# Optimization experiments

Measured on AMD Instinct MI355X. Metric: run time of the kernel, lower is better.

The kernel has to match this reference:

```python
import jax, jax.numpy as jnp
import numpy as np

EPSILON = 0.1      # max offset magnitude relative to anchor norm (init kwarg)
NORM_EPS = 1e-12   # F.normalize denom clamp
DIV_EPS = 1e-8     # offset-norm division eps


def setup_inputs() -> dict:
    key = jax.random.key(0)
    k1, k2 = jax.random.split(key)
    embeddings = jax.random.normal(k1, (4, 2048, 2048), dtype=jnp.float32)
    vocab_embeddings = jax.random.normal(k2, (32000, 2048), dtype=jnp.float32)
    return {"embeddings": embeddings, "vocab_embeddings": vocab_embeddings}


def reference(embeddings, vocab_embeddings):
    B, S, D = embeddings.shape
    x = embeddings.reshape(-1, D)                                   # [BS, D]
    xn = x / jnp.maximum(jnp.linalg.norm(x, axis=-1, keepdims=True), NORM_EPS)
    vn = vocab_embeddings / jnp.maximum(
        jnp.linalg.norm(vocab_embeddings, axis=-1, keepdims=True), NORM_EPS)
    sim = xn @ vn.T                                                 # [BS, V]
    anchor_ids = jnp.argmax(sim, axis=-1)                           # [BS]
    anchor = vocab_embeddings[anchor_ids]                           # [BS, D]
    offset = x - anchor
    offset_norm = jnp.linalg.norm(offset, axis=-1, keepdims=True)
    anchor_norm = jnp.linalg.norm(anchor, axis=-1, keepdims=True)
    scale = jnp.minimum(EPSILON * anchor_norm / (offset_norm + DIV_EPS), 1.0)
    result = anchor + offset * scale
    return result.reshape(B, S, D), anchor_ids.reshape(B, S)
```

## Files before the change

### kernel.cpp

```cpp
#include <hip/hip_runtime.h>
#include <hip/hip_bf16.h>

#define DIM 2048
#define BM 128
#define BN 256
#define BK 64
#define KSTEPS (DIM / BK)
#define A_TILE_BYTES (BM * BK)
#define B_TILE_BYTES (BN * BK)
#define NLEV 8

typedef _Float16 f16x8 __attribute__((ext_vector_type(8)));
typedef float f32x4 __attribute__((ext_vector_type(4)));
typedef int i32x4 __attribute__((ext_vector_type(4)));
typedef unsigned long long u64;

#define INV_SX 27.6f
#define INV_SVN 1150.0f

typedef const unsigned int __attribute__((address_space(1))) gu32;
typedef unsigned int __attribute__((address_space(3))) lu32;

__device__ __forceinline__ void gl_lds16(const void* g, void* l) {
    __builtin_amdgcn_global_load_lds((gu32*)g, (lu32*)l, 16, 0, 0);
}

__device__ __forceinline__ u64 pack_key(float v, unsigned int col) {
    unsigned int b = __float_as_uint(v);
    b ^= (unsigned int)(((int)b >> 31)) | 0x80000000u;
    return ((u64)b << 32) | (u64)(~col);
}
__device__ __forceinline__ u64 pack_key_i(int dot, unsigned int col) {
    unsigned int b = (unsigned int)dot ^ 0x80000000u;
    return ((u64)b << 32) | (u64)(~col);
}
__device__ __forceinline__ u64 umax64(u64 a, u64 b) { return a > b ? a : b; }
__device__ __forceinline__ u64 umin64(u64 a, u64 b) { return a < b ? a : b; }

__device__ __forceinline__ void cascadeN(u64* Rrow, int stride, u64 k) {
    if (k <= Rrow[(NLEV - 1) * stride]) return;
#pragma unroll
    for (int l = 0; l < NLEV; ++l) {
        u64 old = atomicMax(&Rrow[l * stride], k);
        k = umin64(k, old);
        if (!k) return;
    }
}
__device__ __forceinline__ void cascade3(u64* r1, u64* r2, u64* r3, u64 k) {
    u64 old = atomicMax(r1, k);
    k = umin64(k, old);
    if (k) {
        old = atomicMax(r2, k);
        k = umin64(k, old);
        if (k) atomicMax(r3, k);
    }
}

__device__ __forceinline__ int toff(int row, int kg) {
    const int line = row >> 1;
    const int s8 = ((row & 1) << 2) | kg;
    return line * 128 + ((s8 ^ (line & 7)) << 4);
}

__device__ __forceinline__ int swz(int row, int slot) {
    return row * 32 + (slot ^ ((row >> 1) & 3)) * 8;
}

__global__ void vocab_invnorm_kernel(const float* __restrict__ Vg,
                                     float* __restrict__ invnorm) {
    const int v = blockIdx.x;
    const int t = threadIdx.x;
    const float* row = Vg + (size_t)v * DIM;
    float4 f0 = *reinterpret_cast<const float4*>(row + t * 8);
    float4 f1 = *reinterpret_cast<const float4*>(row + t * 8 + 4);
    float s = f0.x*f0.x + f0.y*f0.y + f0.z*f0.z + f0.w*f0.w
            + f1.x*f1.x + f1.y*f1.y + f1.z*f1.z + f1.w*f1.w;
#pragma unroll
    for (int off = 32; off > 0; off >>= 1) s += __shfl_down(s, off);
    __shared__ float ls[4];
    const int lane = t & 63, w = t >> 6;
    if (lane == 0) ls[w] = s;
    __syncthreads();
    if (t == 0) {
        float tot = ls[0] + ls[1] + ls[2] + ls[3];
        invnorm[v] = 1.0f / fmaxf(sqrtf(tot), 1e-12f);
    }
}

__device__ __forceinline__ void q16pack(const float* xv, float s, int* out4) {
#pragma unroll
    for (int g = 0; g < 4; ++g) {
        int p = 0;
#pragma unroll
        for (int e = 0; e < 4; ++e) {
            int q = __float2int_rn(xv[g * 4 + e] * s);
            q = q > 127 ? 127 : (q < -127 ? -127 : q);
            p |= (q & 255) << (e * 8);
        }
        out4[g] = p;
    }
}

__global__ void convert_x_q(const float* __restrict__ X, signed char* __restrict__ Xq) {
    const int tile = blockIdx.x;
    const int mblk = tile >> 5, ks = tile & 31;
    const float* src = X + (size_t)(mblk * BM) * DIM + ks * BK;
    signed char* dst = Xq + (size_t)tile * A_TILE_BYTES;
    const int t = threadIdx.x;
#pragma unroll
    for (int u = 0; u < 2; ++u) {
        const int c = t + u * 256;
        const int line = c >> 3;
        const int s8 = (c & 7) ^ (line & 7);
        const int row = (line << 1) | (s8 >> 2);
        const int cs = s8 & 3;
        const float* s = src + (size_t)row * DIM + cs * 16;
        float xv[16];
        *(float4*)(&xv[0])  = *(const float4*)(s);
        *(float4*)(&xv[4])  = *(const float4*)(s + 4);
        *(float4*)(&xv[8])  = *(const float4*)(s + 8);
        *(float4*)(&xv[12]) = *(const float4*)(s + 12);
        int q4[4];
        q16pack(xv, INV_SX, q4);
        *(int4*)(dst + c * 16) = make_int4(q4[0], q4[1], q4[2], q4[3]);
    }
}

__global__ void convert_v_q(const float* __restrict__ Vg,
                            const float* __restrict__ invnorm,
                            signed char* __restrict__ Vq) {
    const int tile = blockIdx.x;
    const int nblk = tile >> 5, ks = tile & 31;
    const float* src = Vg + (size_t)(nblk * BN) * DIM + ks * BK;
    signed char* dst = Vq + (size_t)tile * B_TILE_BYTES;
    const int t = threadIdx.x;
#pragma unroll
    for (int u = 0; u < 4; ++u) {
        const int c = t + u * 256;
        const int line = c >> 3;
        const int s8 = (c & 7) ^ (line & 7);
        const int row = (line << 1) | (s8 >> 2);
        const int cs = s8 & 3;
        const float sc = invnorm[nblk * BN + row] * INV_SVN;
        const float* s = src + (size_t)row * DIM + cs * 16;
        float xv[16];
        *(float4*)(&xv[0])  = *(const float4*)(s);
        *(float4*)(&xv[4])  = *(const float4*)(s + 4);
        *(float4*)(&xv[8])  = *(const float4*)(s + 8);
        *(float4*)(&xv[12]) = *(const float4*)(s + 12);
        int q4[4];
        q16pack(xv, sc, q4);
        *(int4*)(dst + c * 16) = make_int4(q4[0], q4[1], q4[2], q4[3]);
    }
}

__global__ __launch_bounds__(512, 4) void sim_i8_breg(
        const signed char* __restrict__ Xq, const signed char* __restrict__ Vq,
        u64* __restrict__ R, int M) {
    __shared__ alignas(16) signed char ldsA[2][A_TILE_BYTES];

    const int tid = threadIdx.x;
    const int flat = blockIdx.x;
    const int idx  = (flat & 7) * 1000 + (flat >> 3);
    const int mblk = idx & 63;
    const int nblk = idx >> 6;

    const int lane = tid & 63;
    const int w  = tid >> 6;
    const int wm = w >> 2, wn = w & 3;
    const int lr = lane & 15;
    const int kg = lane >> 4;

    const signed char* Atiles = Xq + (size_t)mblk * KSTEPS * A_TILE_BYTES;
    const signed char* Btiles = Vq + (size_t)nblk * KSTEPS * B_TILE_BYTES;

    i32x4 acc[4][4] = {};

    int offA[4], offB[4];
#pragma unroll
    for (int i = 0; i < 4; ++i) offA[i] = toff(wm * 64 + i * 16 + lr, kg);
#pragma unroll
    for (int j = 0; j < 4; ++j) offB[j] = toff(wn * 64 + j * 16 + lr, kg);

    const int cA = tid * 16;

    gl_lds16(Atiles + cA, &ldsA[0][cA]);
    i32x4 b0 = *(const i32x4*)(Btiles + offB[0]);
    i32x4 b1 = *(const i32x4*)(Btiles + offB[1]);
    i32x4 b2 = *(const i32x4*)(Btiles + offB[2]);
    i32x4 b3 = *(const i32x4*)(Btiles + offB[3]);
    __syncthreads();

    int cur = 0;
    for (int ks = 0; ks < KSTEPS; ++ks) {
        const int nk = (ks + 1 < KSTEPS) ? (ks + 1) : ks;
        const signed char* bn = Btiles + (size_t)nk * B_TILE_BYTES;
        i32x4 nb0 = *(const i32x4*)(bn + offB[0]);
        i32x4 nb1 = *(const i32x4*)(bn + offB[1]);
        i32x4 nb2 = *(const i32x4*)(bn + offB[2]);
        i32x4 nb3 = *(const i32x4*)(bn + offB[3]);
        if (ks + 1 < KSTEPS) {
            const signed char* an = Atiles + (size_t)(ks + 1) * A_TILE_BYTES;
            gl_lds16(an + cA, &ldsA[cur ^ 1][cA]);
        }
#pragma unroll
        for (int i = 0; i < 4; ++i) {
            i32x4 ahf = *(const i32x4*)(&ldsA[cur][offA[i]]);
            acc[i][0] = __builtin_amdgcn_mfma_i32_16x16x64_i8(ahf, b0, acc[i][0], 0, 0, 0);
            acc[i][1] = __builtin_amdgcn_mfma_i32_16x16x64_i8(ahf, b1, acc[i][1], 0, 0, 0);
            acc[i][2] = __builtin_amdgcn_mfma_i32_16x16x64_i8(ahf, b2, acc[i][2], 0, 0, 0);
            acc[i][3] = __builtin_amdgcn_mfma_i32_16x16x64_i8(ahf, b3, acc[i][3], 0, 0, 0);
        }
        __syncthreads();
        b0 = nb0; b1 = nb1; b2 = nb2; b3 = nb3;
        cur ^= 1;
    }

    const int m0 = mblk * BM, n0 = nblk * BN;
#pragma unroll
    for (int i = 0; i < 4; ++i) {
#pragma unroll
        for (int r = 0; r < 4; ++r) {
            u64 k[4];
#pragma unroll
            for (int j = 0; j < 4; ++j)
                k[j] = pack_key_i(acc[i][j][r],
                                  (unsigned int)(n0 + wn * 64 + j * 16 + lr));
            u64 m01 = umax64(k[0], k[1]), n01 = umin64(k[0], k[1]);
            u64 m23 = umax64(k[2], k[3]), n23 = umin64(k[2], k[3]);
            u64 a1k = umax64(m01, m23);
            u64 a2k = umax64(umin64(m01, m23), umax64(n01, n23));
#pragma unroll
            for (int mask = 1; mask < 16; mask <<= 1) {
                u64 o1 = __shfl_xor(a1k, mask);
                u64 o2 = __shfl_xor(a2k, mask);
                u64 t1 = umax64(a1k, o1);
                a2k = umax64(umin64(a1k, o1), umax64(a2k, o2));
                a1k = t1;
            }
            if (lr == 0) {
                const int row = m0 + wm * 64 + i * 16 + kg * 4 + r;
                cascadeN(&R[row], M, a1k);
                cascadeN(&R[row], M, a2k);
            }
        }
    }
}

__global__ __launch_bounds__(256) void sim_coarse_fallback(
        const float* __restrict__ X, const float* __restrict__ Vg,
        const float* __restrict__ invnorm,
        u64* __restrict__ R1, u64* __restrict__ R2, u64* __restrict__ R3) {
    __shared__ alignas(16) _Float16 Ah[128 * 32];
    __shared__ alignas(16) _Float16 Bh[128 * 32];
    const int tid = threadIdx.x;
    const int flat = blockIdx.x;
    const int idx  = (flat & 7) * 2000 + (flat >> 3);
    const int panel = idx / 3200;
    const int w_    = idx - panel * 3200;
    const int mblk  = w_ & 63;
    const int nblk  = panel * 50 + (w_ >> 6);
    const int m0 = mblk * 128, n0 = nblk * 128;
    const int lane = tid & 63;
    const int w  = tid >> 6;
    const int wm = w >> 1, wn = w & 1;
    const int lr = lane & 15;
    const int kg = lane >> 4;
    const int sr  = tid >> 2;
    const int skc = tid & 3;
    const float* Aptr0 = X  + (size_t)(m0 + sr)      * DIM + skc * 8;
    const float* Aptr1 = X  + (size_t)(m0 + 64 + sr) * DIM + skc * 8;
    const float* Bptr0 = Vg + (size_t)(n0 + sr)      * DIM + skc * 8;
    const float* Bptr1 = Vg + (size_t)(n0 + 64 + sr) * DIM + skc * 8;
    float4 ra[4], rb[4];
    ra[0] = *(const float4*)(Aptr0);     ra[1] = *(const float4*)(Aptr0 + 4);
    ra[2] = *(const float4*)(Aptr1);     ra[3] = *(const float4*)(Aptr1 + 4);
    rb[0] = *(const float4*)(Bptr0);     rb[1] = *(const float4*)(Bptr0 + 4);
    rb[2] = *(const float4*)(Bptr1);     rb[3] = *(const float4*)(Bptr1 + 4);
    f32x4 acc[4][4] = {};
    const int wA0 = swz(sr, skc), wA1 = swz(sr + 64, skc);
    for (int ks = 0; ks < 64; ++ks) {
        {
            f16x8 h; float xv[8];
            *(float4*)(&xv[0]) = ra[0]; *(float4*)(&xv[4]) = ra[1];
#pragma unroll
            for (int e = 0; e < 8; ++e) h[e] = (_Float16)xv[e];
            *(f16x8*)(&Ah[wA0]) = h;
            *(float4*)(&xv[0]) = ra[2]; *(float4*)(&xv[4]) = ra[3];
#pragma unroll
            for (int e = 0; e < 8; ++e) h[e] = (_Float16)xv[e];
            *(f16x8*)(&Ah[wA1]) = h;
            *(float4*)(&xv[0]) = rb[0]; *(float4*)(&xv[4]) = rb[1];
#pragma unroll
            for (int e = 0; e < 8; ++e) h[e] = (_Float16)xv[e];
            *(f16x8*)(&Bh[wA0]) = h;
            *(float4*)(&xv[0]) = rb[2]; *(float4*)(&xv[4]) = rb[3];
#pragma unroll
            for (int e = 0; e < 8; ++e) h[e] = (_Float16)xv[e];
            *(f16x8*)(&Bh[wA1]) = h;
        }
        __syncthreads();
        if (ks + 1 < 64) {
            const int ko = (ks + 1) * 32;
            ra[0] = *(const float4*)(Aptr0 + ko); ra[1] = *(const float4*)(Aptr0 + ko + 4);
            ra[2] = *(const float4*)(Aptr1 + ko); ra[3] = *(const float4*)(Aptr1 + ko + 4);
            rb[0] = *(const float4*)(Bptr0 + ko); rb[1] = *(const float4*)(Bptr0 + ko + 4);
            rb[2] = *(const float4*)(Bptr1 + ko); rb[3] = *(const float4*)(Bptr1 + ko + 4);
        }
        f16x8 bhf[4];
#pragma unroll
        for (int j = 0; j < 4; ++j)
            bhf[j] = *(const f16x8*)(&Bh[swz(wn * 64 + j * 16 + lr, kg)]);
#pragma unroll
        for (int i = 0; i < 4; ++i) {
            f16x8 ahf = *(const f16x8*)(&Ah[swz(wm * 64 + i * 16 + lr, kg)]);
#pragma unroll
            for (int j = 0; j < 4; ++j)
                acc[i][j] = __builtin_amdgcn_mfma_f32_16x16x32_f16(ahf, bhf[j], acc[i][j], 0, 0, 0);
        }
        __syncthreads();
    }
    float inv[4];
#pragma unroll
    for (int j = 0; j < 4; ++j) inv[j] = invnorm[n0 + wn * 64 + j * 16 + lr];
#pragma unroll
    for (int i = 0; i < 4; ++i) {
#pragma unroll
        for (int r = 0; r < 4; ++r) {
            u64 k[4];
#pragma unroll
            for (int j = 0; j < 4; ++j)
                k[j] = pack_key(acc[i][j][r] * inv[j],
                                (unsigned int)(n0 + wn * 64 + j * 16 + lr));
            u64 m01 = umax64(k[0], k[1]), n01 = umin64(k[0], k[1]);
            u64 m23 = umax64(k[2], k[3]), n23 = umin64(k[2], k[3]);
            u64 a1 = umax64(m01, m23);
            u64 a2 = umax64(umin64(m01, m23), umax64(n01, n23));
#pragma unroll
            for (int mask = 1; mask < 16; mask <<= 1) {
                u64 b1 = __shfl_xor(a1, mask);
                u64 b2 = __shfl_xor(a2, mask);
                u64 t1 = umax64(a1, b1);
                a2 = umax64(umin64(a1, b1), umax64(a2, b2));
                a1 = t1;
            }
            if (lr == 0) {
                const int row = m0 + wm * 64 + i * 16 + kg * 4 + r;
                cascade3(&R1[row], &R2[row], &R3[row], a1);
                cascade3(&R1[row], &R2[row], &R3[row], a2);
            }
        }
    }
}

__device__ __forceinline__ float block_sum(float v, float* sbuf, int t) {
#pragma unroll
    for (int off = 32; off > 0; off >>= 1) v += __shfl_down(v, off);
    const int lane = t & 63, w = t >> 6;
    __syncthreads();
    if (lane == 0) sbuf[w] = v;
    __syncthreads();
    return sbuf[0] + sbuf[1] + sbuf[2] + sbuf[3];
}

__global__ void rescue_finalize_kernel(const float* __restrict__ X,
                                       const float* __restrict__ Vg,
                                       const u64* __restrict__ R, int M, int NV,
                                       float* __restrict__ outx,
                                       float* __restrict__ outid) {
    const int row = blockIdx.x;
    const int t = threadIdx.x;
    __shared__ float sbuf[4];

    int cand[NLEV];
#pragma unroll
    for (int c = 0; c < NLEV; ++c) {
        unsigned int id = ~(unsigned int)(R[c * M + row] & 0xFFFFFFFFull);
        cand[c] = (id < (unsigned int)NV) ? (int)id : 0;
    }

    const float* x = X + (size_t)row * DIM;
    float4 x0 = *reinterpret_cast<const float4*>(x + t * 8);
    float4 x1 = *reinterpret_cast<const float4*>(x + t * 8 + 4);
    float xxp = x0.x*x0.x + x0.y*x0.y + x0.z*x0.z + x0.w*x0.w
              + x1.x*x1.x + x1.y*x1.y + x1.z*x1.z + x1.w*x1.w;
    const float xx = block_sum(xxp, sbuf, t);
    const float xn = fmaxf(sqrtf(xx), 1e-12f);

    u64 bestkey = 0ull;
    int bestid = cand[0];
    float bestsa = 0.f;
#pragma unroll
    for (int c = 0; c < NLEV; ++c) {
        const float* v = Vg + (size_t)cand[c] * DIM;
        float4 v0 = *reinterpret_cast<const float4*>(v + t * 8);
        float4 v1 = *reinterpret_cast<const float4*>(v + t * 8 + 4);
        float dp = x0.x*v0.x + x0.y*v0.y + x0.z*v0.z + x0.w*v0.w
                 + x1.x*v1.x + x1.y*v1.y + x1.z*v1.z + x1.w*v1.w;
        float vp = v0.x*v0.x + v0.y*v0.y + v0.z*v0.z + v0.w*v0.w
                 + v1.x*v1.x + v1.y*v1.y + v1.z*v1.z + v1.w*v1.w;
        const float dot = block_sum(dp, sbuf, t);
        const float vv  = block_sum(vp, sbuf, t);
        const float s = dot / (xn * fmaxf(sqrtf(vv), 1e-12f));
        u64 key = pack_key(s, (unsigned int)cand[c]);
        if (key > bestkey) { bestkey = key; bestid = cand[c]; bestsa = vv; }
    }

    const float* a = Vg + (size_t)bestid * DIM;
    float4 a0 = *reinterpret_cast<const float4*>(a + t * 8);
    float4 a1 = *reinterpret_cast<const float4*>(a + t * 8 + 4);
    float4 d0 = make_float4(x0.x-a0.x, x0.y-a0.y, x0.z-a0.z, x0.w-a0.w);
    float4 d1 = make_float4(x1.x-a1.x, x1.y-a1.y, x1.z-a1.z, x1.w-a1.w);
    float sop = d0.x*d0.x + d0.y*d0.y + d0.z*d0.z + d0.w*d0.w
              + d1.x*d1.x + d1.y*d1.y + d1.z*d1.z + d1.w*d1.w;
    const float so = block_sum(sop, sbuf, t);
    const float scale = fminf(0.1f * sqrtf(bestsa) / (sqrtf(so) + 1e-8f), 1.0f);

    float4 o0 = make_float4(a0.x + d0.x*scale, a0.y + d0.y*scale,
                            a0.z + d0.z*scale, a0.w + d0.w*scale);
    float4 o1 = make_float4(a1.x + d1.x*scale, a1.y + d1.y*scale,
                            a1.z + d1.z*scale, a1.w + d1.w*scale);
    float* o = outx + (size_t)row * DIM + t * 8;
    *reinterpret_cast<float4*>(o)     = o0;
    *reinterpret_cast<float4*>(o + 4) = o1;
    if (t == 0) outid[row] = (float)bestid;
}

extern "C" void kernel_launch(void* const* d_in, const int* in_sizes, int n_in,
                              void* d_out, int out_size, void* d_ws, size_t ws_size,
                              hipStream_t stream) {
    const float* X  = (const float*)d_in[0];
    const float* Vg = (const float*)d_in[1];
    const int M  = in_sizes[0] / DIM;
    const int NV = in_sizes[1] / DIM;

    char* ws = (char*)d_ws;
    u64* R = (u64*)ws;
    size_t off = (size_t)NLEV * M * sizeof(u64);
    float* invnorm = (float*)(ws + off);
    off += ((size_t)NV * sizeof(float) + 255) & ~255ull;
    signed char* Xq = (signed char*)(ws + off);
    off += (size_t)M * DIM;
    signed char* Vq = (signed char*)(ws + off);
    off += (size_t)NV * DIM;
    const bool fast = (ws_size >= off);

    float* outx  = (float*)d_out;
    float* outid = outx + (size_t)M * DIM;

    hipMemsetAsync(R, 0, (size_t)NLEV * M * sizeof(u64), stream);
    vocab_invnorm_kernel<<<NV, 256, 0, stream>>>(Vg, invnorm);

    if (fast) {
        convert_x_q<<<(M / BM) * KSTEPS, 256, 0, stream>>>(X, Xq);
        convert_v_q<<<(NV / BN) * KSTEPS, 256, 0, stream>>>(Vg, invnorm, Vq);
        dim3 grid((NV / BN) * (M / BM));
        sim_i8_breg<<<grid, 512, 0, stream>>>(Xq, Vq, R, M);
    } else {
        dim3 gridf((NV / 128) * (M / 128));
        sim_coarse_fallback<<<gridf, 256, 0, stream>>>(X, Vg, invnorm,
                                                       R, R + M, R + 2 * M);
    }

    rescue_finalize_kernel<<<M, 256, 0, stream>>>(X, Vg, R, M, NV, outx, outid);
}
```

Measured before the change: 1.298 ms.

## Reshape int8 GEMM tiles to 256x128 with fatter 4-wave blocks

Swaps the block tile so each block covers 256 X rows by 128 vocab columns, using 256 threads (2x2 waves) where each wave computes a 128x64 sub-tile with 8x4 MFMA accumulators. X tiles are streamed through LDS while vocab tiles still go straight to registers, so each register-held B fragment is reused across twice as many MFMAs. The quantisation kernels change their tile layouts to match. The cost is more accumulator registers per thread and fewer waves per block, which lowers occupancy and latency hiding, and the block-index swizzle is left unchanged.

```diff
diff --git a/kernel.cpp b/kernel.cpp
--- a/kernel.cpp
+++ b/kernel.cpp
@@ -2,12 +2,12 @@
 #include <hip/hip_bf16.h>
 
 #define DIM 2048
-#define BM 128
-#define BN 256
+#define BM 256
+#define BN 128
 #define BK 64
 #define KSTEPS (DIM / BK)
-#define A_TILE_BYTES (BM * BK)
-#define B_TILE_BYTES (BN * BK)
+#define XT_BYTES (BM * BK)
+#define VT_BYTES (BN * BK)
 #define NLEV 8
 
 typedef _Float16 f16x8 __attribute__((ext_vector_type(8)));
@@ -105,10 +105,10 @@
     const int tile = blockIdx.x;
     const int mblk = tile >> 5, ks = tile & 31;
     const float* src = X + (size_t)(mblk * BM) * DIM + ks * BK;
-    signed char* dst = Xq + (size_t)tile * A_TILE_BYTES;
+    signed char* dst = Xq + (size_t)tile * XT_BYTES;
     const int t = threadIdx.x;
 #pragma unroll
-    for (int u = 0; u < 2; ++u) {
+    for (int u = 0; u < 4; ++u) {
         const int c = t + u * 256;
         const int line = c >> 3;
         const int s8 = (c & 7) ^ (line & 7);
@@ -132,10 +132,10 @@
     const int tile = blockIdx.x;
     const int nblk = tile >> 5, ks = tile & 31;
     const float* src = Vg + (size_t)(nblk * BN) * DIM + ks * BK;
-    signed char* dst = Vq + (size_t)tile * B_TILE_BYTES;
+    signed char* dst = Vq + (size_t)tile * VT_BYTES;
     const int t = threadIdx.x;
 #pragma unroll
-    for (int u = 0; u < 4; ++u) {
+    for (int u = 0; u < 2; ++u) {
         const int c = t + u * 256;
         const int line = c >> 3;
         const int s8 = (c & 7) ^ (line & 7);
@@ -154,37 +154,41 @@
     }
 }
 
-__global__ __launch_bounds__(512, 4) void sim_i8_breg(
+__global__ __launch_bounds__(256, 2) void sim_i8_fat(
         const signed char* __restrict__ Xq, const signed char* __restrict__ Vq,
         u64* __restrict__ R, int M) {
-    __shared__ alignas(16) signed char ldsA[2][A_TILE_BYTES];
+    __shared__ alignas(16) signed char ldsA[2][XT_BYTES];
 
     const int tid = threadIdx.x;
     const int flat = blockIdx.x;
     const int idx  = (flat & 7) * 1000 + (flat >> 3);
-    const int mblk = idx & 63;
-    const int nblk = idx >> 6;
+    const int mblk = idx & 31;
+    const int nblk = idx >> 5;
 
     const int lane = tid & 63;
     const int w  = tid >> 6;
-    const int wm = w >> 2, wn = w & 3;
+    const int wm = w >> 1, wn = w & 1;
     const int lr = lane & 15;
     const int kg = lane >> 4;
 
-    const signed char* Atiles = Xq + (size_t)mblk * KSTEPS * A_TILE_BYTES;
-    const signed char* Btiles = Vq + (size_t)nblk * KSTEPS * B_TILE_BYTES;
-
-    i32x4 acc[4][4] = {};
-
-    int offA[4], offB[4];
-#pragma unroll
-    for (int i = 0; i < 4; ++i) offA[i] = toff(wm * 64 + i * 16 + lr, kg);
+    const signed char* Atiles = Xq + (size_t)mblk * KSTEPS * XT_BYTES;
+    const signed char* Btiles = Vq + (size_t)nblk * KSTEPS * VT_BYTES;
+
+    i32x4 acc[8][4] = {};
+
+    int offA[8], offB[4];
+#pragma unroll
+    for (int i = 0; i < 8; ++i) offA[i] = toff(wm * 128 + i * 16 + lr, kg);
 #pragma unroll
     for (int j = 0; j < 4; ++j) offB[j] = toff(wn * 64 + j * 16 + lr, kg);
 
-    const int cA = tid * 16;
-
-    gl_lds16(Atiles + cA, &ldsA[0][cA]);
+    const int cA0 = tid * 16, cA1 = (tid + 256) * 16;
+    const int cA2 = (tid + 512) * 16, cA3 = (tid + 768) * 16;
+
+    gl_lds16(Atiles + cA0, &ldsA[0][cA0]);
+    gl_lds16(Atiles + cA1, &ldsA[0][cA1]);
+    gl_lds16(Atiles + cA2, &ldsA[0][cA2]);
+    gl_lds16(Atiles + cA3, &ldsA[0][cA3]);
     i32x4 b0 = *(const i32x4*)(Btiles + offB[0]);
     i32x4 b1 = *(const i32x4*)(Btiles + offB[1]);
     i32x4 b2 = *(const i32x4*)(Btiles + offB[2]);
@@ -194,17 +198,20 @@
     int cur = 0;
     for (int ks = 0; ks < KSTEPS; ++ks) {
         const int nk = (ks + 1 < KSTEPS) ? (ks + 1) : ks;
-        const signed char* bn = Btiles + (size_t)nk * B_TILE_BYTES;
+        const signed char* bn = Btiles + (size_t)nk * VT_BYTES;
         i32x4 nb0 = *(const i32x4*)(bn + offB[0]);
         i32x4 nb1 = *(const i32x4*)(bn + offB[1]);
         i32x4 nb2 = *(const i32x4*)(bn + offB[2]);
         i32x4 nb3 = *(const i32x4*)(bn + offB[3]);
         if (ks + 1 < KSTEPS) {
-            const signed char* an = Atiles + (size_t)(ks + 1) * A_TILE_BYTES;
-            gl_lds16(an + cA, &ldsA[cur ^ 1][cA]);
-        }
-#pragma unroll
-        for (int i = 0; i < 4; ++i) {
+            const signed char* an = Atiles + (size_t)(ks + 1) * XT_BYTES;
+            gl_lds16(an + cA0, &ldsA[cur ^ 1][cA0]);
+            gl_lds16(an + cA1, &ldsA[cur ^ 1][cA1]);
+            gl_lds16(an + cA2, &ldsA[cur ^ 1][cA2]);
+            gl_lds16(an + cA3, &ldsA[cur ^ 1][cA3]);
+        }
+#pragma unroll
+        for (int i = 0; i < 8; ++i) {
             i32x4 ahf = *(const i32x4*)(&ldsA[cur][offA[i]]);
             acc[i][0] = __builtin_amdgcn_mfma_i32_16x16x64_i8(ahf, b0, acc[i][0], 0, 0, 0);
             acc[i][1] = __builtin_amdgcn_mfma_i32_16x16x64_i8(ahf, b1, acc[i][1], 0, 0, 0);
@@ -218,7 +225,7 @@
 
     const int m0 = mblk * BM, n0 = nblk * BN;
 #pragma unroll
-    for (int i = 0; i < 4; ++i) {
+    for (int i = 0; i < 8; ++i) {
 #pragma unroll
         for (int r = 0; r < 4; ++r) {
             u64 k[4];
@@ -226,10 +233,10 @@
             for (int j = 0; j < 4; ++j)
                 k[j] = pack_key_i(acc[i][j][r],
                                   (unsigned int)(n0 + wn * 64 + j * 16 + lr));
-            u64 m01 = umax64(k[0], k[1]), n01 = umin64(k[0], k[1]);
-            u64 m23 = umax64(k[2], k[3]), n23 = umin64(k[2], k[3]);
+            u64 m01 = umax64(k[0], k[1]), q01 = umin64(k[0], k[1]);
+            u64 m23 = umax64(k[2], k[3]), q23 = umin64(k[2], k[3]);
             u64 a1k = umax64(m01, m23);
-            u64 a2k = umax64(umin64(m01, m23), umax64(n01, n23));
+            u64 a2k = umax64(umin64(m01, m23), umax64(q01, q23));
 #pragma unroll
             for (int mask = 1; mask < 16; mask <<= 1) {
                 u64 o1 = __shfl_xor(a1k, mask);
@@ -239,7 +246,7 @@
                 a1k = t1;
             }
             if (lr == 0) {
-                const int row = m0 + wm * 64 + i * 16 + kg * 4 + r;
+                const int row = m0 + wm * 128 + i * 16 + kg * 4 + r;
                 cascadeN(&R[row], M, a1k);
                 cascadeN(&R[row], M, a2k);
             }
@@ -455,7 +462,7 @@
         convert_x_q<<<(M / BM) * KSTEPS, 256, 0, stream>>>(X, Xq);
         convert_v_q<<<(NV / BN) * KSTEPS, 256, 0, stream>>>(Vg, invnorm, Vq);
         dim3 grid((NV / BN) * (M / BM));
-        sim_i8_breg<<<grid, 512, 0, stream>>>(Xq, Vq, R, M);
+        sim_i8_fat<<<grid, 256, 0, stream>>>(Xq, Vq, R, M);
     } else {
         dim3 gridf((NV / 128) * (M / 128));
         sim_coarse_fallback<<<gridf, 256, 0, stream>>>(X, Vg, invnorm,
```

Result: slower. 1.584 ms (+22.1%).

## Use four-slot LDS ring with prefetch depth two and one barrier per step

Applied to the files above, without the earlier changes.

Replaces the double-buffered A tile in LDS with a four-slot ring that prefetches two k-steps ahead, using explicit vmcnt waits and a single barrier per iteration instead of two syncthreads. The goal is to hide global-to-LDS latency and halve barrier overhead in the int8 MFMA similarity GEMM. LDS use doubles to 32KB per block, which could limit occupancy at four blocks per CU. The hand-picked vmcnt count must match the actual number of outstanding loads, or tiles could be read before they arrive.

```diff
diff --git a/kernel.cpp b/kernel.cpp
--- a/kernel.cpp
+++ b/kernel.cpp
@@ -154,10 +154,10 @@
     }
 }
 
-__global__ __launch_bounds__(512, 4) void sim_i8_breg(
+__global__ __launch_bounds__(512, 4) void sim_i8_ring(
         const signed char* __restrict__ Xq, const signed char* __restrict__ Vq,
         u64* __restrict__ R, int M) {
-    __shared__ alignas(16) signed char ldsA[2][A_TILE_BYTES];
+    __shared__ alignas(16) signed char ldsA[4][A_TILE_BYTES];
 
     const int tid = threadIdx.x;
     const int flat = blockIdx.x;
@@ -184,36 +184,39 @@
 
     const int cA = tid * 16;
 
-    gl_lds16(Atiles + cA, &ldsA[0][cA]);
+    gl_lds16(Atiles + cA,                &ldsA[0][cA]);
+    gl_lds16(Atiles + A_TILE_BYTES + cA, &ldsA[1][cA]);
     i32x4 b0 = *(const i32x4*)(Btiles + offB[0]);
     i32x4 b1 = *(const i32x4*)(Btiles + offB[1]);
     i32x4 b2 = *(const i32x4*)(Btiles + offB[2]);
     i32x4 b3 = *(const i32x4*)(Btiles + offB[3]);
-    __syncthreads();
-
-    int cur = 0;
+    asm volatile("s_waitcnt vmcnt(0)" ::: "memory");
+    __builtin_amdgcn_s_barrier();
+    __builtin_amdgcn_sched_barrier(0);
+
     for (int ks = 0; ks < KSTEPS; ++ks) {
-        const int nk = (ks + 1 < KSTEPS) ? (ks + 1) : ks;
+        const int nk = (ks + 1 < KSTEPS) ? (ks + 1) : (KSTEPS - 1);
         const signed char* bn = Btiles + (size_t)nk * B_TILE_BYTES;
         i32x4 nb0 = *(const i32x4*)(bn + offB[0]);
         i32x4 nb1 = *(const i32x4*)(bn + offB[1]);
         i32x4 nb2 = *(const i32x4*)(bn + offB[2]);
         i32x4 nb3 = *(const i32x4*)(bn + offB[3]);
-        if (ks + 1 < KSTEPS) {
-            const signed char* an = Atiles + (size_t)(ks + 1) * A_TILE_BYTES;
-            gl_lds16(an + cA, &ldsA[cur ^ 1][cA]);
-        }
+        const int ak = (ks + 2 < KSTEPS) ? (ks + 2) : (KSTEPS - 1);
+        gl_lds16(Atiles + (size_t)ak * A_TILE_BYTES + cA, &ldsA[(ks + 2) & 3][cA]);
+        asm volatile("s_waitcnt vmcnt(9)" ::: "memory");
+        __builtin_amdgcn_s_barrier();
+        __builtin_amdgcn_sched_barrier(0);
+
+        const signed char* As = &ldsA[ks & 3][0];
 #pragma unroll
         for (int i = 0; i < 4; ++i) {
-            i32x4 ahf = *(const i32x4*)(&ldsA[cur][offA[i]]);
+            i32x4 ahf = *(const i32x4*)(As + offA[i]);
             acc[i][0] = __builtin_amdgcn_mfma_i32_16x16x64_i8(ahf, b0, acc[i][0], 0, 0, 0);
             acc[i][1] = __builtin_amdgcn_mfma_i32_16x16x64_i8(ahf, b1, acc[i][1], 0, 0, 0);
             acc[i][2] = __builtin_amdgcn_mfma_i32_16x16x64_i8(ahf, b2, acc[i][2], 0, 0, 0);
             acc[i][3] = __builtin_amdgcn_mfma_i32_16x16x64_i8(ahf, b3, acc[i][3], 0, 0, 0);
         }
-        __syncthreads();
         b0 = nb0; b1 = nb1; b2 = nb2; b3 = nb3;
-        cur ^= 1;
     }
 
     const int m0 = mblk * BM, n0 = nblk * BN;
@@ -226,10 +229,10 @@
             for (int j = 0; j < 4; ++j)
                 k[j] = pack_key_i(acc[i][j][r],
                                   (unsigned int)(n0 + wn * 64 + j * 16 + lr));
-            u64 m01 = umax64(k[0], k[1]), n01 = umin64(k[0], k[1]);
-            u64 m23 = umax64(k[2], k[3]), n23 = umin64(k[2], k[3]);
+            u64 m01 = umax64(k[0], k[1]), q01 = umin64(k[0], k[1]);
+            u64 m23 = umax64(k[2], k[3]), q23 = umin64(k[2], k[3]);
             u64 a1k = umax64(m01, m23);
-            u64 a2k = umax64(umin64(m01, m23), umax64(n01, n23));
+            u64 a2k = umax64(umin64(m01, m23), umax64(q01, q23));
 #pragma unroll
             for (int mask = 1; mask < 16; mask <<= 1) {
                 u64 o1 = __shfl_xor(a1k, mask);
@@ -455,7 +458,7 @@
         convert_x_q<<<(M / BM) * KSTEPS, 256, 0, stream>>>(X, Xq);
         convert_v_q<<<(NV / BN) * KSTEPS, 256, 0, stream>>>(Vg, invnorm, Vq);
         dim3 grid((NV / BN) * (M / BM));
-        sim_i8_breg<<<grid, 512, 0, stream>>>(Xq, Vq, R, M);
+        sim_i8_ring<<<grid, 512, 0, stream>>>(Xq, Vq, R, M);
     } else {
         dim3 gridf((NV / 128) * (M / 128));
         sim_coarse_fallback<<<gridf, 256, 0, stream>>>(X, Vg, invnorm,
```

After: 1.238 ms. 4.6% less time.
